# Kernel tuning notes

Measured on AMD Instinct MI355X. Metric: run time of the kernel, lower is better.

## Reference

```python
import jax, jax.numpy as jnp
import numpy as np

N_EMBD = 1024
N_HEADS = 16
HEAD_DIM = N_EMBD // N_HEADS


def setup_inputs() -> dict:
    key = jax.random.key(0)
    ks = jax.random.split(key, 6)
    s = 1.0 / np.sqrt(N_EMBD)
    x = jax.random.normal(ks[0], (2, 2048, N_EMBD), dtype=jnp.float32)
    # torch Linear weights are [out, in]; y = x @ W.T
    Wk = jax.random.uniform(ks[1], (N_EMBD, N_EMBD), jnp.float32, -s, s)
    Wq = jax.random.uniform(ks[2], (N_EMBD, N_EMBD), jnp.float32, -s, s)
    Wv = jax.random.uniform(ks[3], (N_EMBD, N_EMBD), jnp.float32, -s, s)
    Wp = jax.random.uniform(ks[4], (N_EMBD, N_EMBD), jnp.float32, -s, s)
    bp = jax.random.uniform(ks[5], (N_EMBD,), jnp.float32, -s, s)
    return {"x": x, "Wq": Wq, "Wk": Wk, "Wv": Wv, "Wp": Wp, "bp": bp}


def reference(x, Wq, Wk, Wv, Wp, bp):
    B, T, C = x.shape
    H, D = N_HEADS, HEAD_DIM
    # projections (torch Linear: x @ W.T), reshape to [B, H, T, D]
    q = (x @ Wq.T).reshape(B, T, H, D).transpose(0, 2, 1, 3)
    k = (x @ Wk.T).reshape(B, T, H, D).transpose(0, 2, 1, 3)
    v = (x @ Wv.T).reshape(B, T, H, D).transpose(0, 2, 1, 3)
    # scaled causal attention, full [B,H,T,T] scores (faithful to original)
    att = jnp.einsum('bhqd,bhkd->bhqk', q, k) * (D ** -0.5)
    causal = jnp.tril(jnp.ones((T, T), dtype=bool))
    att = jnp.where(causal[None, None], att, -jnp.inf)
    att = jax.nn.softmax(att, axis=-1)
    out = jnp.einsum('bhqk,bhkd->bhqd', att, v)
    out = out.transpose(0, 2, 1, 3).reshape(B, T, C)
    return out @ Wp.T + bp
```

## Files before the change

kernel.cpp:

```cpp
#include <hip/hip_runtime.h>

typedef __bf16 bf16;
typedef __bf16 bf16x8 __attribute__((ext_vector_type(8)));
typedef float f32x4 __attribute__((ext_vector_type(4)));

typedef __attribute__((address_space(1))) const void as1_void;
typedef __attribute__((address_space(3))) void as3_void;

#define DEV __device__ __forceinline__
#define NEG_BIG (-1.0e30f)


DEV void async_load16(const void* g, void* l) {
  __builtin_amdgcn_global_load_lds((as1_void*)g, (as3_void*)l, 16, 0, 0);
}
DEV bf16x8 load8(const bf16* p) { bf16x8 v; __builtin_memcpy(&v, p, 16); return v; }
DEV void store8(bf16* p, bf16x8 v) { __builtin_memcpy(p, &v, 16); }

DEV int sniff_bf16(const unsigned short* __restrict__ xr) {
  const int lane = threadIdx.x & 63;
  const unsigned short w = xr[lane * 2];
  const int e = (w >> 7) & 0xFF;
  const bool sane = ((w & 0x7FFF) == 0) || (e >= 97 && e <= 157);
  return __popcll(__ballot(sane)) >= 48;
}

struct ConvArgs {
  const void* src[6];
  bf16* dst[6];
  int n[6];
};

__global__ __launch_bounds__(256) void convert_kernel(ConvArgs a) {
  const int isbf = sniff_bf16((const unsigned short*)a.src[0]);
  const int t = blockIdx.y;
  const int n = a.n[t];
  bf16* d = a.dst[t];
  const int stride = gridDim.x * 256 * 8;
  if (isbf) {
    const bf16* s = (const bf16*)a.src[t];
    for (int i = (blockIdx.x * 256 + threadIdx.x) * 8; i < n; i += stride)
      store8(d + i, load8(s + i));
  } else {
    const float* s = (const float*)a.src[t];
    for (int i = (blockIdx.x * 256 + threadIdx.x) * 8; i < n; i += stride) {
      float tmp[8];
      __builtin_memcpy(tmp, s + i, 32);
      bf16x8 v;
#pragma unroll
      for (int j = 0; j < 8; ++j) v[j] = (bf16)tmp[j];
      store8(d + i, v);
    }
  }
}

DEV void gemm_core_128_p(const bf16* A, const bf16* W, const int K, int m0, int n0,
                         f32x4 (&acc)[4][4]) {
  __shared__ alignas(16) bf16 As[3][128 * 32];
  __shared__ alignas(16) bf16 Bs[3][128 * 32];
  const int tid = threadIdx.x;
  const int lane = tid & 63;
  const int wid = tid >> 6;
  const int wm = (wid >> 1) << 6;
  const int wn = (wid & 1) << 6;
  const int lr = lane & 15;
  const int lg = lane >> 4;

  size_t srcA[2], srcB[2];
  int ldsoff[2];
#pragma unroll
  for (int it = 0; it < 2; ++it) {
    const int lin = it * 256 + tid;
    const int lr2 = lin >> 3, c = lin & 7;
    const int u = c ^ (lr2 & 7);
    const int r = lr2 * 2 + (u >> 2);
    const int g = u & 3;
    srcA[it] = (size_t)(m0 + r) * K + (size_t)(g * 8);
    srcB[it] = (size_t)(n0 + r) * K + (size_t)(g * 8);
    ldsoff[it] = lin * 8;
  }
  int offA[4], offB[4];
#pragma unroll
  for (int i = 0; i < 4; ++i) {
    const int r = wm + i * 16 + lr;
    const int cc = (lg | ((r & 1) << 2)) ^ ((r >> 1) & 7);
    offA[i] = (((r >> 1) << 3) | cc) * 8;
  }
#pragma unroll
  for (int j = 0; j < 4; ++j) {
    const int r = wn + j * 16 + lr;
    const int cc = (lg | ((r & 1) << 2)) ^ ((r >> 1) & 7);
    offB[j] = (((r >> 1) << 3) | cc) * 8;
  }

  const f32x4 zero = {0.f, 0.f, 0.f, 0.f};
#pragma unroll
  for (int i = 0; i < 4; ++i)
#pragma unroll
    for (int j = 0; j < 4; ++j) acc[i][j] = zero;

  const int nt = K >> 5;

  auto stage = [&](int buf, int t) {
    const size_t k0 = (size_t)(t << 5);
#pragma unroll
    for (int it = 0; it < 2; ++it) {
      async_load16(A + srcA[it] + k0, &As[buf][0] + ldsoff[it]);
      async_load16(W + srcB[it] + k0, &Bs[buf][0] + ldsoff[it]);
    }
  };

  auto compute = [&](int buf) {
    const bf16* as = &As[buf][0];
    const bf16* bs = &Bs[buf][0];
    bf16x8 af[4], bfr[4];
#pragma unroll
    for (int i = 0; i < 4; ++i) af[i] = load8(as + offA[i]);
#pragma unroll
    for (int j = 0; j < 4; ++j) bfr[j] = load8(bs + offB[j]);
    __builtin_amdgcn_s_setprio(1);
#pragma unroll
    for (int i = 0; i < 4; ++i)
#pragma unroll
      for (int j = 0; j < 4; ++j)
        acc[i][j] = __builtin_amdgcn_mfma_f32_16x16x32_bf16(af[i], bfr[j], acc[i][j], 0, 0, 0);
    __builtin_amdgcn_s_setprio(0);
  };

  stage(0, 0);
  stage(1, 1);
  int b0 = 0, b1 = 1, b2 = 2;
  for (int t = 0; t < nt; ++t) {
    if (t + 1 < nt) asm volatile("s_waitcnt vmcnt(4)" ::: "memory");
    else            asm volatile("s_waitcnt vmcnt(0)" ::: "memory");
    __builtin_amdgcn_s_barrier();
    if (t + 2 < nt) stage(b2, t + 2);
    compute(b0);
    const int tmp = b0; b0 = b1; b1 = b2; b2 = tmp;
  }
}

DEV size_t frag_idx(int row, int col) {
  return ((size_t)(((col >> 5) * 4 + ((row >> 4) & 3)) * 64 + ((col >> 3) & 3) * 16 + (row & 15)) << 3)
         | (size_t)(col & 7);
}

__global__ __launch_bounds__(256) void qkv_proj_kernel(
    const bf16* __restrict__ x, const bf16* __restrict__ Wq,
    const bf16* __restrict__ Wk, const bf16* __restrict__ Wv,
    bf16* __restrict__ q_ws, bf16* __restrict__ k_ws, bf16* __restrict__ vt_ws) {
  const int L = blockIdx.x;
  const int xcd = L & 7;
  const int i2 = L >> 3;
  const int m0 = (xcd * 4 + (i2 & 3)) << 7;
  const int rest = i2 >> 2;
  const int n0 = (rest & 7) << 7;
  const int mode = rest >> 3;
  const bf16* W = (mode == 0) ? Wq : (mode == 1) ? Wk : Wv;
  f32x4 acc[4][4];
  gemm_core_128_p(x, W, 1024, m0, n0, acc);

  const int tid = threadIdx.x;
  const int lane = tid & 63, wid = tid >> 6;
  const int wm = (wid >> 1) << 6, wn = (wid & 1) << 6;
  const int lr = lane & 15, lg = lane >> 4;
  bf16* out = (mode == 0) ? q_ws : (mode == 1) ? k_ws : vt_ws;
#pragma unroll
  for (int i = 0; i < 4; ++i) {
#pragma unroll
    for (int r = 0; r < 4; ++r) {
      const int m = m0 + wm + i * 16 + lg * 4 + r;
      const int b = m >> 11, t = m & 2047;
#pragma unroll
      for (int j = 0; j < 4; ++j) {
        const int n = n0 + wn + j * 16 + lr;
        const int h = n >> 6, d = n & 63;
        const float v = acc[i][j][r];
        const size_t base = ((size_t)(b * 16 + h) << 17) + ((size_t)(t >> 6) << 12);
        const size_t idx = base + ((mode < 2) ? frag_idx(t & 63, d) : frag_idx(d, t & 63));
        out[idx] = (bf16)v;
      }
    }
  }
}

__global__ __launch_bounds__(256, 2) void attn_kernel(
    const bf16* __restrict__ q_ws, const bf16* __restrict__ k_ws,
    const bf16* __restrict__ vt_ws, bf16* __restrict__ a_ws) {
  const int L = blockIdx.x;
  const int xcd = L & 7;
  const int bh = xcd * 4 + ((L >> 3) & 3);
  const int qt = 31 - (L >> 5);
  const int tid = threadIdx.x;
  const int lane = tid & 63, w = tid >> 6;
  const int lr = lane & 15, lg = lane >> 4;
  const int fo = lg * 16 + lr;

  __shared__ alignas(16) bf16 Ks[3][4096];
  __shared__ alignas(16) bf16 Vs[3][4096];
  __shared__ alignas(16) bf16 Ps[4][16 * 72];
  bf16* ps = &Ps[w][0];

  const size_t hb = (size_t)bh << 17;
  const int b = bh >> 4, h = bh & 15;
  const f32x4 zero = {0.f, 0.f, 0.f, 0.f};

  const size_t qtb = hb + ((size_t)qt << 12);
  const bf16* kbase = k_ws + hb;
  const bf16* vbase = vt_ws + hb;

  bf16x8 aq[2];
#pragma unroll
  for (int c2 = 0; c2 < 2; ++c2)
    aq[c2] = load8(q_ws + qtb + (size_t)(((c2 * 4 + w) * 64 + fo) << 3));

  f32x4 o_acc[4];
#pragma unroll
  for (int j = 0; j < 4; ++j) o_acc[j] = zero;
  float lsum[4] = {0.f, 0.f, 0.f, 0.f};

  const int nt = qt + 1;
  auto ktof = [&](int s) { return (s == 0) ? qt : (s - 1); };

  auto stage = [&](int buf, int s) {
    const int kt = ktof(s);
    const bf16* kg = kbase + ((size_t)kt << 12);
    const bf16* vg = vbase + ((size_t)kt << 12);
#pragma unroll
    for (int it = 0; it < 2; ++it) {
      const int lin = it * 256 + tid;
      async_load16(kg + lin * 8, &Ks[buf][0] + lin * 8);
      async_load16(vg + lin * 8, &Vs[buf][0] + lin * 8);
    }
  };

  auto step = [&](int buf, bool diag) {
    const bf16* ks = &Ks[buf][0];
    const bf16* vs = &Vs[buf][0];
    f32x4 s[4];
    __builtin_amdgcn_s_setprio(1);
#pragma unroll
    for (int j = 0; j < 4; ++j) {
      s[j] = __builtin_amdgcn_mfma_f32_16x16x32_bf16(
          aq[0], load8(ks + (size_t)(((0 * 4 + j) * 64 + fo) << 3)), zero, 0, 0, 0);
      s[j] = __builtin_amdgcn_mfma_f32_16x16x32_bf16(
          aq[1], load8(ks + (size_t)(((1 * 4 + j) * 64 + fo) << 3)), s[j], 0, 0, 0);
    }
    __builtin_amdgcn_s_setprio(0);
    float p[4][4];
#pragma unroll
    for (int j = 0; j < 4; ++j) {
#pragma unroll
      for (int r = 0; r < 4; ++r) {
        float v = s[j][r] * 0.125f;
        if (diag && (j * 16 + lr) > (w * 16 + lg * 4 + r)) v = NEG_BIG;
        p[j][r] = __expf(v);
      }
    }
#pragma unroll
    for (int r = 0; r < 4; ++r)
      lsum[r] += (p[0][r] + p[1][r]) + (p[2][r] + p[3][r]);
#pragma unroll
    for (int j = 0; j < 4; ++j)
#pragma unroll
      for (int r = 0; r < 4; ++r)
        ps[(lg * 4 + r) * 72 + j * 16 + lr] = (bf16)p[j][r];
    __builtin_amdgcn_s_setprio(1);
#pragma unroll
    for (int c2 = 0; c2 < 2; ++c2) {
      const bf16x8 ap = load8(ps + lr * 72 + c2 * 32 + lg * 8);
#pragma unroll
      for (int j = 0; j < 4; ++j)
        o_acc[j] = __builtin_amdgcn_mfma_f32_16x16x32_bf16(
            ap, load8(vs + (size_t)(((c2 * 4 + j) * 64 + fo) << 3)), o_acc[j], 0, 0, 0);
    }
    __builtin_amdgcn_s_setprio(0);
  };

  stage(0, 0);
  if (nt > 1) stage(1, 1);
  int b0 = 0, b1 = 1, b2 = 2;
  for (int t = 0; t < nt; ++t) {
    if (t + 1 < nt) asm volatile("s_waitcnt vmcnt(4)" ::: "memory");
    else            asm volatile("s_waitcnt vmcnt(0)" ::: "memory");
    __builtin_amdgcn_s_barrier();
    if (t + 2 < nt) stage(b2, t + 2);
    step(b0, t == 0);
    const int tmp = b0; b0 = b1; b1 = b2; b2 = tmp;
  }

  float l_i[4];
#pragma unroll
  for (int r = 0; r < 4; ++r) {
    float v = lsum[r];
#pragma unroll
    for (int off = 1; off < 16; off <<= 1) v += __shfl_xor(v, off, 64);
    l_i[r] = v;
  }

#pragma unroll
  for (int r = 0; r < 4; ++r) {
    const int t = qt * 64 + w * 16 + lg * 4 + r;
    const float inv = 1.f / l_i[r];
#pragma unroll
    for (int j = 0; j < 4; ++j) {
      const size_t idx = (((size_t)(b * 2048 + t)) << 10) | (size_t)(h * 64 + j * 16 + lr);
      a_ws[idx] = (bf16)(o_acc[j][r] * inv);
    }
  }
}

__global__ __launch_bounds__(256) void out_proj_kernel(
    const bf16* __restrict__ A, const bf16* __restrict__ Wp,
    const bf16* __restrict__ bp, void* __restrict__ out,
    const unsigned short* __restrict__ xraw) {
  const int L = blockIdx.x;
  const int xcd = L & 7;
  const int i2 = L >> 3;
  const int m0 = (xcd * 4 + (i2 & 3)) << 7;
  const int n0 = (i2 >> 2) << 7;
  f32x4 acc[4][4];
  gemm_core_128_p(A, Wp, 1024, m0, n0, acc);

  const int tid = threadIdx.x;
  const int lane = tid & 63, wid = tid >> 6;
  const int wm = (wid >> 1) << 6, wn = (wid & 1) << 6;
  const int lr = lane & 15, lg = lane >> 4;
  const int isbf = sniff_bf16(xraw);
#pragma unroll
  for (int i = 0; i < 4; ++i) {
#pragma unroll
    for (int r = 0; r < 4; ++r) {
      const int m = m0 + wm + i * 16 + lg * 4 + r;
#pragma unroll
      for (int j = 0; j < 4; ++j) {
        const int n = n0 + wn + j * 16 + lr;
        const float v = acc[i][j][r] + (float)bp[n];
        const size_t idx = ((size_t)m << 10) | (size_t)n;
        if (isbf) ((bf16*)out)[idx] = (bf16)v;
        else      ((float*)out)[idx] = v;
      }
    }
  }
}

extern "C" void kernel_launch(void* const* d_in, const int* in_sizes, int n_in,
                              void* d_out, int out_size, void* d_ws, size_t ws_size,
                              hipStream_t stream) {
  (void)in_sizes; (void)n_in; (void)out_size;
  if (ws_size < (50u << 20)) return;

  char* ws = (char*)d_ws;
  bf16* q_ws  = (bf16*)(ws);
  bf16* k_ws  = (bf16*)(ws + (8u << 20));
  bf16* vt_ws = (bf16*)(ws + (16u << 20));
  bf16* a_ws  = (bf16*)(ws + (24u << 20));
  bf16* xc    = (bf16*)(ws + (32u << 20));
  bf16* Wqc   = (bf16*)(ws + (40u << 20));
  bf16* Wkc   = (bf16*)(ws + (42u << 20));
  bf16* Wvc   = (bf16*)(ws + (44u << 20));
  bf16* Wpc   = (bf16*)(ws + (46u << 20));
  bf16* bpc   = (bf16*)(ws + (48u << 20));

  ConvArgs ca;
  ca.src[0] = d_in[0]; ca.dst[0] = xc;  ca.n[0] = 4096 * 1024;
  ca.src[1] = d_in[1]; ca.dst[1] = Wqc; ca.n[1] = 1024 * 1024;
  ca.src[2] = d_in[2]; ca.dst[2] = Wkc; ca.n[2] = 1024 * 1024;
  ca.src[3] = d_in[3]; ca.dst[3] = Wvc; ca.n[3] = 1024 * 1024;
  ca.src[4] = d_in[4]; ca.dst[4] = Wpc; ca.n[4] = 1024 * 1024;
  ca.src[5] = d_in[5]; ca.dst[5] = bpc; ca.n[5] = 1024;
  convert_kernel<<<dim3(512, 6), 256, 0, stream>>>(ca);

  qkv_proj_kernel<<<768, 256, 0, stream>>>(xc, Wqc, Wkc, Wvc, q_ws, k_ws, vt_ws);
  attn_kernel<<<1024, 256, 0, stream>>>(q_ws, k_ws, vt_ws, a_ws);
  out_proj_kernel<<<256, 256, 0, stream>>>(a_ws, Wpc, bpc, d_out,
                                           (const unsigned short*)d_in[0]);
}
```

Baseline: 184.9 us.

## Rework QKV GEMM A-path, fold softmax scale into Q, retile out-proj and attention buffering

The QKV GEMM now loads A fragments straight from global memory into registers and keeps only B staged in LDS, with two register sets alternating. The softmax scale times log2(e) is folded into Q at projection time so attention can use a raw v_exp_f32 instead of a multiply plus __expf. Attention drops from triple to double buffering with full vmcnt waits, which frees LDS so occupancy hints rise to 3. The output projection moves to 128x64 tiles with twice as many blocks to fill more CUs. The risks are less load/compute overlap in attention and uncoalesced direct A loads in the QKV GEMM.

```diff
diff --git a/kernel.cpp b/kernel.cpp
--- a/kernel.cpp
+++ b/kernel.cpp
@@ -16,6 +16,7 @@
 }
 DEV bf16x8 load8(const bf16* p) { bf16x8 v; __builtin_memcpy(&v, p, 16); return v; }
 DEV void store8(bf16* p, bf16x8 v) { __builtin_memcpy(p, &v, 16); }
+DEV float fexp2(float x) { float r; asm("v_exp_f32 %0, %1" : "=v"(r) : "v"(x)); return r; }
 
 DEV int sniff_bf16(const unsigned short* __restrict__ xr) {
   const int lane = threadIdx.x & 63;
@@ -54,9 +55,8 @@
   }
 }
 
-DEV void gemm_core_128_p(const bf16* A, const bf16* W, const int K, int m0, int n0,
-                         f32x4 (&acc)[4][4]) {
-  __shared__ alignas(16) bf16 As[3][128 * 32];
+DEV void gemm_core_128_ad(const bf16* A, const bf16* W, const int K, int m0, int n0,
+                          f32x4 (&acc)[4][4]) {
   __shared__ alignas(16) bf16 Bs[3][128 * 32];
   const int tid = threadIdx.x;
   const int lane = tid & 63;
@@ -66,7 +66,7 @@
   const int lr = lane & 15;
   const int lg = lane >> 4;
 
-  size_t srcA[2], srcB[2];
+  size_t srcB[2];
   int ldsoff[2];
 #pragma unroll
   for (int it = 0; it < 2; ++it) {
@@ -75,11 +75,108 @@
     const int u = c ^ (lr2 & 7);
     const int r = lr2 * 2 + (u >> 2);
     const int g = u & 3;
-    srcA[it] = (size_t)(m0 + r) * K + (size_t)(g * 8);
     srcB[it] = (size_t)(n0 + r) * K + (size_t)(g * 8);
     ldsoff[it] = lin * 8;
   }
-  int offA[4], offB[4];
+  int offB[4];
+#pragma unroll
+  for (int j = 0; j < 4; ++j) {
+    const int r = wn + j * 16 + lr;
+    const int cc = (lg | ((r & 1) << 2)) ^ ((r >> 1) & 7);
+    offB[j] = (((r >> 1) << 3) | cc) * 8;
+  }
+  const bf16* pa[4];
+#pragma unroll
+  for (int i = 0; i < 4; ++i)
+    pa[i] = A + (size_t)(m0 + wm + i * 16 + lr) * K + (size_t)(lg * 8);
+
+  const f32x4 zero = {0.f, 0.f, 0.f, 0.f};
+#pragma unroll
+  for (int i = 0; i < 4; ++i)
+#pragma unroll
+    for (int j = 0; j < 4; ++j) acc[i][j] = zero;
+
+  const int nt = K >> 5;
+
+  auto stageB = [&](int buf, int t) {
+    const size_t k0 = (size_t)(t << 5);
+#pragma unroll
+    for (int it = 0; it < 2; ++it)
+      async_load16(W + srcB[it] + k0, &Bs[buf][0] + ldsoff[it]);
+  };
+  auto loadA = [&](bf16x8 (&af)[4], int t) {
+    const int k0 = t << 5;
+#pragma unroll
+    for (int i = 0; i < 4; ++i) af[i] = load8(pa[i] + k0);
+  };
+  auto compute = [&](int buf, const bf16x8 (&af)[4]) {
+    const bf16* bs = &Bs[buf][0];
+    bf16x8 bfr[4];
+#pragma unroll
+    for (int j = 0; j < 4; ++j) bfr[j] = load8(bs + offB[j]);
+    __builtin_amdgcn_s_setprio(1);
+#pragma unroll
+    for (int i = 0; i < 4; ++i)
+#pragma unroll
+      for (int j = 0; j < 4; ++j)
+        acc[i][j] = __builtin_amdgcn_mfma_f32_16x16x32_bf16(af[i], bfr[j], acc[i][j], 0, 0, 0);
+    __builtin_amdgcn_s_setprio(0);
+  };
+
+  bf16x8 afA[4], afB[4];
+  stageB(0, 0);
+  loadA(afA, 0);
+  stageB(1, 1);
+  loadA(afB, 1);
+  int b0 = 0, b1 = 1, b2 = 2;
+  for (int t = 0; t < nt; t += 2) {
+    if (t + 1 < nt) asm volatile("s_waitcnt vmcnt(6)" ::: "memory");
+    else            asm volatile("s_waitcnt vmcnt(0)" ::: "memory");
+    __builtin_amdgcn_s_barrier();
+    if (t + 2 < nt) stageB(b2, t + 2);
+    compute(b0, afA);
+    if (t + 2 < nt) loadA(afA, t + 2);
+    { const int tmp = b0; b0 = b1; b1 = b2; b2 = tmp; }
+    if (t + 2 < nt) asm volatile("s_waitcnt vmcnt(6)" ::: "memory");
+    else            asm volatile("s_waitcnt vmcnt(0)" ::: "memory");
+    __builtin_amdgcn_s_barrier();
+    if (t + 3 < nt) stageB(b2, t + 3);
+    compute(b0, afB);
+    if (t + 3 < nt) loadA(afB, t + 3);
+    { const int tmp = b0; b0 = b1; b1 = b2; b2 = tmp; }
+  }
+}
+
+DEV void gemm_core_128x64_p(const bf16* A, const bf16* W, const int K, int m0, int n0,
+                            f32x4 (&acc)[4][2]) {
+  __shared__ alignas(16) bf16 As[3][128 * 32];
+  __shared__ alignas(16) bf16 Bs[3][64 * 32];
+  const int tid = threadIdx.x;
+  const int lane = tid & 63;
+  const int wid = tid >> 6;
+  const int wm = (wid >> 1) << 6;
+  const int wn = (wid & 1) << 5;
+  const int lr = lane & 15;
+  const int lg = lane >> 4;
+
+  size_t srcA[2], srcB;
+  int ldsoffA[2], ldsoffB;
+#pragma unroll
+  for (int it = 0; it < 2; ++it) {
+    const int lin = it * 256 + tid;
+    const int lr2 = lin >> 3, c = lin & 7;
+    const int u = c ^ (lr2 & 7);
+    srcA[it] = (size_t)(m0 + lr2 * 2 + (u >> 2)) * K + (size_t)((u & 3) * 8);
+    ldsoffA[it] = lin * 8;
+  }
+  {
+    const int lin = tid;
+    const int lr2 = lin >> 3, c = lin & 7;
+    const int u = c ^ (lr2 & 7);
+    srcB = (size_t)(n0 + lr2 * 2 + (u >> 2)) * K + (size_t)((u & 3) * 8);
+    ldsoffB = lin * 8;
+  }
+  int offA[4], offB[2];
 #pragma unroll
   for (int i = 0; i < 4; ++i) {
     const int r = wm + i * 16 + lr;
@@ -87,7 +184,7 @@
     offA[i] = (((r >> 1) << 3) | cc) * 8;
   }
 #pragma unroll
-  for (int j = 0; j < 4; ++j) {
+  for (int j = 0; j < 2; ++j) {
     const int r = wn + j * 16 + lr;
     const int cc = (lg | ((r & 1) << 2)) ^ ((r >> 1) & 7);
     offB[j] = (((r >> 1) << 3) | cc) * 8;
@@ -97,32 +194,31 @@
 #pragma unroll
   for (int i = 0; i < 4; ++i)
 #pragma unroll
-    for (int j = 0; j < 4; ++j) acc[i][j] = zero;
+    for (int j = 0; j < 2; ++j) acc[i][j] = zero;
 
   const int nt = K >> 5;
 
   auto stage = [&](int buf, int t) {
     const size_t k0 = (size_t)(t << 5);
 #pragma unroll
-    for (int it = 0; it < 2; ++it) {
-      async_load16(A + srcA[it] + k0, &As[buf][0] + ldsoff[it]);
-      async_load16(W + srcB[it] + k0, &Bs[buf][0] + ldsoff[it]);
-    }
+    for (int it = 0; it < 2; ++it)
+      async_load16(A + srcA[it] + k0, &As[buf][0] + ldsoffA[it]);
+    async_load16(W + srcB + k0, &Bs[buf][0] + ldsoffB);
   };
 
   auto compute = [&](int buf) {
     const bf16* as = &As[buf][0];
     const bf16* bs = &Bs[buf][0];
-    bf16x8 af[4], bfr[4];
+    bf16x8 af[4], bfr[2];
 #pragma unroll
     for (int i = 0; i < 4; ++i) af[i] = load8(as + offA[i]);
 #pragma unroll
-    for (int j = 0; j < 4; ++j) bfr[j] = load8(bs + offB[j]);
+    for (int j = 0; j < 2; ++j) bfr[j] = load8(bs + offB[j]);
     __builtin_amdgcn_s_setprio(1);
 #pragma unroll
     for (int i = 0; i < 4; ++i)
 #pragma unroll
-      for (int j = 0; j < 4; ++j)
+      for (int j = 0; j < 2; ++j)
         acc[i][j] = __builtin_amdgcn_mfma_f32_16x16x32_bf16(af[i], bfr[j], acc[i][j], 0, 0, 0);
     __builtin_amdgcn_s_setprio(0);
   };
@@ -131,7 +227,7 @@
   stage(1, 1);
   int b0 = 0, b1 = 1, b2 = 2;
   for (int t = 0; t < nt; ++t) {
-    if (t + 1 < nt) asm volatile("s_waitcnt vmcnt(4)" ::: "memory");
+    if (t + 1 < nt) asm volatile("s_waitcnt vmcnt(3)" ::: "memory");
     else            asm volatile("s_waitcnt vmcnt(0)" ::: "memory");
     __builtin_amdgcn_s_barrier();
     if (t + 2 < nt) stage(b2, t + 2);
@@ -145,7 +241,7 @@
          | (size_t)(col & 7);
 }
 
-__global__ __launch_bounds__(256) void qkv_proj_kernel(
+__global__ __launch_bounds__(256, 3) void qkv_proj_kernel(
     const bf16* __restrict__ x, const bf16* __restrict__ Wq,
     const bf16* __restrict__ Wk, const bf16* __restrict__ Wv,
     bf16* __restrict__ q_ws, bf16* __restrict__ k_ws, bf16* __restrict__ vt_ws) {
@@ -158,13 +254,14 @@
   const int mode = rest >> 3;
   const bf16* W = (mode == 0) ? Wq : (mode == 1) ? Wk : Wv;
   f32x4 acc[4][4];
-  gemm_core_128_p(x, W, 1024, m0, n0, acc);
+  gemm_core_128_ad(x, W, 1024, m0, n0, acc);
 
   const int tid = threadIdx.x;
   const int lane = tid & 63, wid = tid >> 6;
   const int wm = (wid >> 1) << 6, wn = (wid & 1) << 6;
   const int lr = lane & 15, lg = lane >> 4;
   bf16* out = (mode == 0) ? q_ws : (mode == 1) ? k_ws : vt_ws;
+  const float scale = (mode == 0) ? 0.18033688011112042f : 1.0f;
 #pragma unroll
   for (int i = 0; i < 4; ++i) {
 #pragma unroll
@@ -175,7 +272,7 @@
       for (int j = 0; j < 4; ++j) {
         const int n = n0 + wn + j * 16 + lr;
         const int h = n >> 6, d = n & 63;
-        const float v = acc[i][j][r];
+        const float v = acc[i][j][r] * scale;
         const size_t base = ((size_t)(b * 16 + h) << 17) + ((size_t)(t >> 6) << 12);
         const size_t idx = base + ((mode < 2) ? frag_idx(t & 63, d) : frag_idx(d, t & 63));
         out[idx] = (bf16)v;
@@ -184,30 +281,28 @@
   }
 }
 
-__global__ __launch_bounds__(256, 2) void attn_kernel(
+__global__ __launch_bounds__(256, 3) void attn_kernel(
     const bf16* __restrict__ q_ws, const bf16* __restrict__ k_ws,
     const bf16* __restrict__ vt_ws, bf16* __restrict__ a_ws) {
   const int L = blockIdx.x;
-  const int xcd = L & 7;
-  const int bh = xcd * 4 + ((L >> 3) & 3);
+  const int bh = (L & 7) * 4 + ((L >> 3) & 3);
   const int qt = 31 - (L >> 5);
   const int tid = threadIdx.x;
   const int lane = tid & 63, w = tid >> 6;
   const int lr = lane & 15, lg = lane >> 4;
   const int fo = lg * 16 + lr;
 
-  __shared__ alignas(16) bf16 Ks[3][4096];
-  __shared__ alignas(16) bf16 Vs[3][4096];
+  __shared__ alignas(16) bf16 Ks[2][4096];
+  __shared__ alignas(16) bf16 Vs[2][4096];
   __shared__ alignas(16) bf16 Ps[4][16 * 72];
   bf16* ps = &Ps[w][0];
 
   const size_t hb = (size_t)bh << 17;
   const int b = bh >> 4, h = bh & 15;
   const f32x4 zero = {0.f, 0.f, 0.f, 0.f};
-
-  const size_t qtb = hb + ((size_t)qt << 12);
   const bf16* kbase = k_ws + hb;
   const bf16* vbase = vt_ws + hb;
+  const size_t qtb = hb + ((size_t)qt << 12);
 
   bf16x8 aq[2];
 #pragma unroll
@@ -252,9 +347,9 @@
     for (int j = 0; j < 4; ++j) {
 #pragma unroll
       for (int r = 0; r < 4; ++r) {
-        float v = s[j][r] * 0.125f;
+        float v = s[j][r];
         if (diag && (j * 16 + lr) > (w * 16 + lg * 4 + r)) v = NEG_BIG;
-        p[j][r] = __expf(v);
+        p[j][r] = fexp2(v);
       }
     }
 #pragma unroll
@@ -278,30 +373,22 @@
   };
 
   stage(0, 0);
-  if (nt > 1) stage(1, 1);
-  int b0 = 0, b1 = 1, b2 = 2;
+  int cur = 0;
   for (int t = 0; t < nt; ++t) {
-    if (t + 1 < nt) asm volatile("s_waitcnt vmcnt(4)" ::: "memory");
-    else            asm volatile("s_waitcnt vmcnt(0)" ::: "memory");
+    asm volatile("s_waitcnt vmcnt(0)" ::: "memory");
     __builtin_amdgcn_s_barrier();
-    if (t + 2 < nt) stage(b2, t + 2);
-    step(b0, t == 0);
-    const int tmp = b0; b0 = b1; b1 = b2; b2 = tmp;
-  }
-
-  float l_i[4];
+    if (t + 1 < nt) stage(cur ^ 1, t + 1);
+    step(cur, t == 0);
+    cur ^= 1;
+  }
+
 #pragma unroll
   for (int r = 0; r < 4; ++r) {
     float v = lsum[r];
 #pragma unroll
     for (int off = 1; off < 16; off <<= 1) v += __shfl_xor(v, off, 64);
-    l_i[r] = v;
-  }
-
-#pragma unroll
-  for (int r = 0; r < 4; ++r) {
+    const float inv = 1.f / v;
     const int t = qt * 64 + w * 16 + lg * 4 + r;
-    const float inv = 1.f / l_i[r];
 #pragma unroll
     for (int j = 0; j < 4; ++j) {
       const size_t idx = (((size_t)(b * 2048 + t)) << 10) | (size_t)(h * 64 + j * 16 + lr);
@@ -318,13 +405,13 @@
   const int xcd = L & 7;
   const int i2 = L >> 3;
   const int m0 = (xcd * 4 + (i2 & 3)) << 7;
-  const int n0 = (i2 >> 2) << 7;
-  f32x4 acc[4][4];
-  gemm_core_128_p(A, Wp, 1024, m0, n0, acc);
+  const int n0 = (i2 >> 2) << 6;
+  f32x4 acc[4][2];
+  gemm_core_128x64_p(A, Wp, 1024, m0, n0, acc);
 
   const int tid = threadIdx.x;
   const int lane = tid & 63, wid = tid >> 6;
-  const int wm = (wid >> 1) << 6, wn = (wid & 1) << 6;
+  const int wm = (wid >> 1) << 6, wn = (wid & 1) << 5;
   const int lr = lane & 15, lg = lane >> 4;
   const int isbf = sniff_bf16(xraw);
 #pragma unroll
@@ -333,7 +420,7 @@
     for (int r = 0; r < 4; ++r) {
       const int m = m0 + wm + i * 16 + lg * 4 + r;
 #pragma unroll
-      for (int j = 0; j < 4; ++j) {
+      for (int j = 0; j < 2; ++j) {
         const int n = n0 + wn + j * 16 + lr;
         const float v = acc[i][j][r] + (float)bp[n];
         const size_t idx = ((size_t)m << 10) | (size_t)n;
@@ -373,6 +460,6 @@
 
   qkv_proj_kernel<<<768, 256, 0, stream>>>(xc, Wqc, Wkc, Wvc, q_ws, k_ws, vt_ws);
   attn_kernel<<<1024, 256, 0, stream>>>(q_ws, k_ws, vt_ws, a_ws);
-  out_proj_kernel<<<256, 256, 0, stream>>>(a_ws, Wpc, bpc, d_out,
+  out_proj_kernel<<<512, 256, 0, stream>>>(a_ws, Wpc, bpc, d_out,
                                            (const unsigned short*)d_in[0]);
 }
```

New measurement: 200.7 us. 8.5% more time.
